# Optimization experiments

Hardware: AMD Instinct MI355X
Metric: run time of the kernel (lower is better)

## Reference

```python
import jax, jax.numpy as jnp
import numpy as np

N_NODES = 20000
N_EDGES = 320000
N_GRAPHS = 128


def gat_conv(x, W, attn_l, attn_r, bias, src, dst, num_nodes):
    """DGL-style GATConv: per-edge attention, edge softmax over incoming
    edges of each destination node, scatter-sum aggregation."""
    H, D = attn_l.shape
    feat = (x @ W).reshape(-1, H, D)                      # [N,H,D]
    el = jnp.sum(feat * attn_l, axis=-1)                  # [N,H]
    er = jnp.sum(feat * attn_r, axis=-1)                  # [N,H]
    e = jax.nn.leaky_relu(el[src] + er[dst], 0.2)         # [E,H]
    # numerically stable segment softmax over dst
    m = jax.ops.segment_max(e, dst, num_segments=num_nodes)   # [N,H]
    e_exp = jnp.exp(e - m[dst])                               # [E,H]
    denom = jax.ops.segment_sum(e_exp, dst, num_segments=num_nodes)
    alpha = e_exp / denom[dst]                                 # [E,H]
    msg = alpha[:, :, None] * feat[src]                        # [E,H,D]
    rst = jax.ops.segment_sum(msg, dst, num_segments=num_nodes)  # [N,H,D]
    return rst + bias.reshape(1, H, D)


def setup_inputs() -> dict:
    key = jax.random.key(0)
    ks = jax.random.split(key, 12)
    s1 = 1.0 / np.sqrt(256.0)
    s2 = 1.0 / np.sqrt(512.0)
    return {
        "x": jax.random.normal(ks[0], (N_NODES, 256), dtype=jnp.float32),
        "W1": jax.random.normal(ks[1], (256, 512), dtype=jnp.float32) * s1,
        "a_l1": jax.random.normal(ks[2], (8, 64), dtype=jnp.float32) * 0.1,
        "a_r1": jax.random.normal(ks[3], (8, 64), dtype=jnp.float32) * 0.1,
        "b1": jnp.zeros((512,), dtype=jnp.float32),
        "W2": jax.random.normal(ks[4], (512, 128), dtype=jnp.float32) * s2,
        "a_l2": jax.random.normal(ks[5], (1, 128), dtype=jnp.float32) * 0.1,
        "a_r2": jax.random.normal(ks[6], (1, 128), dtype=jnp.float32) * 0.1,
        "b2": jnp.zeros((128,), dtype=jnp.float32),
        "edge_src": jax.random.randint(ks[7], (N_EDGES,), 0, N_NODES, dtype=jnp.int32),
        "edge_dst": jax.random.randint(ks[8], (N_EDGES,), 0, N_NODES, dtype=jnp.int32),
        "graph_ids": jnp.sort(jax.random.randint(ks[9], (N_NODES,), 0, N_GRAPHS, dtype=jnp.int32)),
    }


def reference(x, W1, a_l1, a_r1, b1, W2, a_l2, a_r2, b2, edge_src, edge_dst, graph_ids):
    h = gat_conv(x, W1, a_l1, a_r1, b1, edge_src, edge_dst, N_NODES)  # [N,8,64]
    h = h.reshape(N_NODES, -1)                                        # flatten(1)
    h = gat_conv(h, W2, a_l2, a_r2, b2, edge_src, edge_dst, N_NODES)  # [N,1,128]
    # dgl.mean_nodes: per-graph mean pooling
    ones = jnp.ones((N_NODES,), dtype=h.dtype)
    counts = jax.ops.segment_sum(ones, graph_ids, num_segments=N_GRAPHS)
    sums = jax.ops.segment_sum(h, graph_ids, num_segments=N_GRAPHS)   # [G,1,128]
    hg = sums / jnp.maximum(counts, 1.0)[:, None, None]
    return hg
```

## Files before the change

kernel.cpp:

```cpp
#include <hip/hip_runtime.h>
#include <hip/hip_fp16.h>

#define N_NODES  20000
#define N_EDGES  320000
#define N_GRAPHS 128

typedef _Float16 half8 __attribute__((ext_vector_type(8)));
typedef float    f32x4 __attribute__((ext_vector_type(4)));

__global__ void setup_hist(const float* __restrict__ W1, const float* __restrict__ W2,
                           __half* __restrict__ w1t, __half* __restrict__ w2t,
                           const int* __restrict__ gid, int* __restrict__ gstart,
                           const int* __restrict__ dst, int* __restrict__ deg) {
    const int tid  = blockIdx.x * blockDim.x + threadIdx.x;
    const int nthr = gridDim.x * blockDim.x;
    for (int i = tid; i < 256 * 512; i += nthr) {
        int r = i >> 9, c = i & 511;
        w1t[c * 256 + r] = __float2half(W1[i]);
    }
    for (int i = tid; i < 512 * 128; i += nthr) {
        int r = i >> 7, c = i & 127;
        w2t[c * 512 + r] = __float2half(W2[i]);
    }
    if (tid <= N_GRAPHS) {
        if (tid == N_GRAPHS) gstart[N_GRAPHS] = N_NODES;
        else {
            int lo = 0, hi = N_NODES;
            while (lo < hi) {
                int mid = (lo + hi) >> 1;
                if (gid[mid] < tid) lo = mid + 1; else hi = mid;
            }
            gstart[tid] = lo;
        }
    }
    for (int e = tid; e < N_EDGES; e += nthr) atomicAdd(&deg[dst[e]], 1);
}

__global__ void scan_kernel(const int* __restrict__ deg, int* __restrict__ rowptr, int n) {
    __shared__ int partial[1024];
    const int t = threadIdx.x;
    const int CH = (n + 1023) / 1024;
    const int base = t * CH;
    int local = 0;
    for (int i = 0; i < CH; ++i)
        if (base + i < n) local += deg[base + i];
    partial[t] = local;
    __syncthreads();
    for (int o = 1; o < 1024; o <<= 1) {
        int v = (t >= o) ? partial[t - o] : 0;
        __syncthreads();
        partial[t] += v;
        __syncthreads();
    }
    int run = (t == 0) ? 0 : partial[t - 1];
    for (int i = 0; i < CH; ++i) {
        if (base + i <= n) rowptr[base + i] = run;
        if (base + i < n) run += deg[base + i];
    }
}

template <int BM, int BN, int WM, int WN, int H, int D, bool AF32>
__device__ __forceinline__ void gemm_body(
        int bx, int by,
        const void* __restrict__ A_, const __half* __restrict__ BT,
        __half* __restrict__ C, const float* __restrict__ al,
        const float* __restrict__ ar, float* __restrict__ el,
        float* __restrict__ er, int Mm, int Nn, int Kk) {
    constexpr int BK  = 32;
    constexpr int MFR = WM / 16, NFR = WN / 16;
    constexpr int WCOLS = BN / WN;
    __shared__ __align__(16) __half As[BM * BK];
    __shared__ __align__(16) __half Bs[BN * BK];
    const int tid  = threadIdx.x;
    const int w    = tid >> 6, lane = tid & 63;
    const int wr   = w / WCOLS, wc = w % WCOLS;
    const int brow = bx * BM;
    const int bcol = by * BN;
    const int lr   = lane & 15;
    const int lk   = (lane >> 4) * 8;

    f32x4 acc[MFR][NFR] = {};

    for (int k0 = 0; k0 < Kk; k0 += BK) {
        for (int c = tid; c < BM * 4; c += 256) {
            int r = c >> 2, ko = (c & 3) * 8;
            int gr = brow + r; if (gr >= Mm) gr = Mm - 1;
            int off = (r * BK + ko) ^ ((r & 7) << 3);
            if constexpr (AF32) {
                const float* ap = (const float*)A_ + (size_t)gr * Kk + k0 + ko;
                float4 v0 = *reinterpret_cast<const float4*>(ap);
                float4 v1 = *reinterpret_cast<const float4*>(ap + 4);
                union { __half2 h2[4]; uint4 u; } pk;
                pk.h2[0] = __floats2half2_rn(v0.x, v0.y);
                pk.h2[1] = __floats2half2_rn(v0.z, v0.w);
                pk.h2[2] = __floats2half2_rn(v1.x, v1.y);
                pk.h2[3] = __floats2half2_rn(v1.z, v1.w);
                *reinterpret_cast<uint4*>(&As[off]) = pk.u;
            } else {
                *reinterpret_cast<uint4*>(&As[off]) =
                    *reinterpret_cast<const uint4*>((const __half*)A_ + (size_t)gr * Kk + k0 + ko);
            }
        }
        for (int c = tid; c < BN * 4; c += 256) {
            int r = c >> 2, ko = (c & 3) * 8;
            int off = (r * BK + ko) ^ ((r & 7) << 3);
            *reinterpret_cast<uint4*>(&Bs[off]) =
                *reinterpret_cast<const uint4*>(&BT[(size_t)(bcol + r) * Kk + k0 + ko]);
        }
        __syncthreads();
        half8 af[MFR], bf[NFR];
#pragma unroll
        for (int m = 0; m < MFR; ++m) {
            int r = wr * WM + m * 16 + lr;
            af[m] = *reinterpret_cast<const half8*>(&As[(r * BK + lk) ^ ((r & 7) << 3)]);
        }
#pragma unroll
        for (int n = 0; n < NFR; ++n) {
            int r = wc * WN + n * 16 + lr;
            bf[n] = *reinterpret_cast<const half8*>(&Bs[(r * BK + lk) ^ ((r & 7) << 3)]);
        }
#pragma unroll
        for (int m = 0; m < MFR; ++m)
#pragma unroll
            for (int n = 0; n < NFR; ++n)
                acc[m][n] = __builtin_amdgcn_mfma_f32_16x16x32_f16(af[m], bf[n], acc[m][n], 0, 0, 0);
        __syncthreads();
    }

#pragma unroll
    for (int m = 0; m < MFR; ++m) {
        int r0 = brow + wr * WM + m * 16 + ((lane >> 4) << 2);
#pragma unroll
        for (int n = 0; n < NFR; ++n) {
            int cc = bcol + wc * WN + n * 16 + lr;
#pragma unroll
            for (int g = 0; g < 4; ++g)
                if (r0 + g < Mm) C[(size_t)(r0 + g) * Nn + cc] = __float2half(acc[m][n][g]);
        }
    }
    const int h = (bcol + wc * WN) / D;
    float alv[NFR], arv[NFR];
#pragma unroll
    for (int n = 0; n < NFR; ++n) {
        alv[n] = al[bcol + wc * WN + n * 16 + lr];
        arv[n] = ar[bcol + wc * WN + n * 16 + lr];
    }
#pragma unroll
    for (int m = 0; m < MFR; ++m) {
#pragma unroll
        for (int g = 0; g < 4; ++g) {
            float pl = 0.f, pr = 0.f;
#pragma unroll
            for (int n = 0; n < NFR; ++n) {
                pl += acc[m][n][g] * alv[n];
                pr += acc[m][n][g] * arv[n];
            }
            pl += __shfl_xor(pl, 1); pl += __shfl_xor(pl, 2);
            pl += __shfl_xor(pl, 4); pl += __shfl_xor(pl, 8);
            pr += __shfl_xor(pr, 1); pr += __shfl_xor(pr, 2);
            pr += __shfl_xor(pr, 4); pr += __shfl_xor(pr, 8);
            int gr = brow + wr * WM + m * 16 + ((lane >> 4) << 2) + g;
            if (lr == 0 && gr < Mm) {
                if constexpr (WN == D) {
                    el[(size_t)gr * H + h] = pl;
                    er[(size_t)gr * H + h] = pr;
                } else {
                    atomicAdd(&el[(size_t)gr * H + h], pl);
                    atomicAdd(&er[(size_t)gr * H + h], pr);
                }
            }
        }
    }
}

template <int BM, int BN, int WM, int WN, int H, int D, bool AF32>
__global__ __launch_bounds__(256) void gemm_kernel(
        const void* __restrict__ A_, const __half* __restrict__ BT,
        __half* __restrict__ C, const float* __restrict__ al,
        const float* __restrict__ ar, float* __restrict__ el,
        float* __restrict__ er, int Mm, int Nn, int Kk) {
    gemm_body<BM, BN, WM, WN, H, D, AF32>(blockIdx.x, blockIdx.y, A_, BT, C,
                                          al, ar, el, er, Mm, Nn, Kk);
}

template <int BM, int BN, int WM, int WN, int H, int D, bool AF32>
__global__ __launch_bounds__(256) void gemm_scatter_kernel(
        const void* __restrict__ A_, const __half* __restrict__ BT,
        __half* __restrict__ C, const float* __restrict__ al,
        const float* __restrict__ ar, float* __restrict__ el,
        float* __restrict__ er, int Mm, int Nn, int Kk, int gemmRows,
        const int* __restrict__ src, const int* __restrict__ dst,
        const int* __restrict__ rowptr, int* __restrict__ cursor,
        int* __restrict__ esrc) {
    const int nbGemm = gemmRows * (Nn / BN);
    if ((int)blockIdx.x < nbGemm) {
        gemm_body<BM, BN, WM, WN, H, D, AF32>(blockIdx.x % gemmRows, blockIdx.x / gemmRows,
                                              A_, BT, C, al, ar, el, er, Mm, Nn, Kk);
    } else {
        int e = (blockIdx.x - nbGemm) * blockDim.x + threadIdx.x;
        if (e < N_EDGES) {
            int d = dst[e];
            int pos = rowptr[d] + atomicAdd(&cursor[d], 1);
            esrc[pos] = src[e];
        }
    }
}

template <int F, int H, bool HOUT>
__global__ __launch_bounds__(256) void node_aggr_wave(
        const __half* __restrict__ feat, const float* __restrict__ el,
        const float* __restrict__ er, const int* __restrict__ rowptr,
        const int* __restrict__ esrc, const float* __restrict__ bias,
        void* __restrict__ rst_, int N) {
    constexpr int LPN = F / 8;
    constexpr int NPW = 64 / LPN;
    constexpr int D   = F / H;
    const int wid  = (blockIdx.x * blockDim.x + threadIdx.x) >> 6;
    const int lane = threadIdx.x & 63;
    const int n    = wid * NPW + lane / LPN;
    if (n >= N) return;
    const int col = (lane % LPN) * 8;
    const int h   = col / D;
    const float ern = er[(size_t)n * H + h];
    const int rs = rowptr[n], re = rowptr[n + 1];
    const __half* fq = feat + col;

    float acc[8] = {};
    float dsum = 0.f;
    int i = rs;
    for (; i + 4 <= re; i += 4) {
        int s0 = esrc[i], s1 = esrc[i + 1], s2 = esrc[i + 2], s3 = esrc[i + 3];
        float x0 = el[(size_t)s0 * H + h] + ern;
        float x1 = el[(size_t)s1 * H + h] + ern;
        float x2 = el[(size_t)s2 * H + h] + ern;
        float x3 = el[(size_t)s3 * H + h] + ern;
        x0 = (x0 > 0.f) ? x0 : 0.2f * x0;
        x1 = (x1 > 0.f) ? x1 : 0.2f * x1;
        x2 = (x2 > 0.f) ? x2 : 0.2f * x2;
        x3 = (x3 > 0.f) ? x3 : 0.2f * x3;
        float w0 = __expf(x0), w1 = __expf(x1), w2 = __expf(x2), w3 = __expf(x3);
        union { uint4 u; __half2 h2[4]; } r0, r1, r2, r3;
        r0.u = *reinterpret_cast<const uint4*>(fq + (size_t)s0 * F);
        r1.u = *reinterpret_cast<const uint4*>(fq + (size_t)s1 * F);
        r2.u = *reinterpret_cast<const uint4*>(fq + (size_t)s2 * F);
        r3.u = *reinterpret_cast<const uint4*>(fq + (size_t)s3 * F);
        dsum += (w0 + w1) + (w2 + w3);
#pragma unroll
        for (int k = 0; k < 4; ++k) {
            float2 f0 = __half22float2(r0.h2[k]);
            float2 f1 = __half22float2(r1.h2[k]);
            float2 f2 = __half22float2(r2.h2[k]);
            float2 f3 = __half22float2(r3.h2[k]);
            acc[2 * k]     += w0 * f0.x + w1 * f1.x + w2 * f2.x + w3 * f3.x;
            acc[2 * k + 1] += w0 * f0.y + w1 * f1.y + w2 * f2.y + w3 * f3.y;
        }
    }
    for (; i < re; ++i) {
        int s = esrc[i];
        float x = el[(size_t)s * H + h] + ern;
        x = (x > 0.f) ? x : 0.2f * x;
        float w = __expf(x);
        union { uint4 u; __half2 h2[4]; } r;
        r.u = *reinterpret_cast<const uint4*>(fq + (size_t)s * F);
        dsum += w;
#pragma unroll
        for (int k = 0; k < 4; ++k) {
            float2 f = __half22float2(r.h2[k]);
            acc[2 * k]     += w * f.x;
            acc[2 * k + 1] += w * f.y;
        }
    }
    float inv = (re > rs) ? 1.f / dsum : 0.f;
    float4 b0 = *reinterpret_cast<const float4*>(bias + col);
    float4 b1 = *reinterpret_cast<const float4*>(bias + col + 4);
    float o[8] = {acc[0] * inv + b0.x, acc[1] * inv + b0.y,
                  acc[2] * inv + b0.z, acc[3] * inv + b0.w,
                  acc[4] * inv + b1.x, acc[5] * inv + b1.y,
                  acc[6] * inv + b1.z, acc[7] * inv + b1.w};
    if constexpr (HOUT) {
        union { __half2 h2[4]; uint4 u; } pk;
        pk.h2[0] = __floats2half2_rn(o[0], o[1]);
        pk.h2[1] = __floats2half2_rn(o[2], o[3]);
        pk.h2[2] = __floats2half2_rn(o[4], o[5]);
        pk.h2[3] = __floats2half2_rn(o[6], o[7]);
        *reinterpret_cast<uint4*>((__half*)rst_ + (size_t)n * F + col) = pk.u;
    } else {
        float* op = (float*)rst_ + (size_t)n * F + col;
        *reinterpret_cast<float4*>(op)     = make_float4(o[0], o[1], o[2], o[3]);
        *reinterpret_cast<float4*>(op + 4) = make_float4(o[4], o[5], o[6], o[7]);
    }
}

__global__ __launch_bounds__(1024) void seg_pool_kernel(
        const float* __restrict__ h, const int* __restrict__ start,
        float* __restrict__ out, int D) {
    __shared__ float part[7][128];
    int g = blockIdx.x;
    int d = threadIdx.x & 127;
    int j = threadIdx.x >> 7;
    int s = start[g], e = start[g + 1];
    float acc = 0.f;
    for (int n = s + j; n < e; n += 8) acc += h[(size_t)n * D + d];
    if (j > 0) part[j - 1][d] = acc;
    __syncthreads();
    if (j == 0) {
#pragma unroll
        for (int k = 0; k < 7; ++k) acc += part[k][d];
        out[(size_t)g * D + d] = acc / fmaxf((float)(e - s), 1.f);
    }
}

extern "C" void kernel_launch(void* const* d_in, const int* in_sizes, int n_in,
                              void* d_out, int out_size, void* d_ws, size_t ws_size,
                              hipStream_t stream) {
    const float* x   = (const float*)d_in[0];
    const float* W1  = (const float*)d_in[1];
    const float* al1 = (const float*)d_in[2];
    const float* ar1 = (const float*)d_in[3];
    const float* b1  = (const float*)d_in[4];
    const float* W2  = (const float*)d_in[5];
    const float* al2 = (const float*)d_in[6];
    const float* ar2 = (const float*)d_in[7];
    const float* b2  = (const float*)d_in[8];
    const int* src   = (const int*)d_in[9];
    const int* dst   = (const int*)d_in[10];
    const int* gid   = (const int*)d_in[11];
    float* out = (float*)d_out;

    float* ws = (float*)d_ws;
    size_t off = 0;
    int* deg    = (int*)(ws + off); off += N_NODES;
    int* cursor = (int*)(ws + off); off += N_NODES;
    int* rowptr = (int*)(ws + off); off += N_NODES + 4;
    int* gstart = (int*)(ws + off); off += N_GRAPHS + 4;
    int* esrc   = (int*)(ws + off); off += N_EDGES;
    __half* w1t    = (__half*)(ws + off); off += 512 * 256 / 2;
    __half* w2t    = (__half*)(ws + off); off += 128 * 512 / 2;
    __half* feat1h = (__half*)(ws + off); off += (size_t)N_NODES * 256;
    float*  el1    = ws + off; off += (size_t)N_NODES * 8;
    float*  er1    = ws + off; off += (size_t)N_NODES * 8;
    __half* rst1h  = (__half*)(ws + off); off += (size_t)N_NODES * 256;
    __half* feat2h = (__half*)(ws + off); off += (size_t)N_NODES * 64;
    float*  el2    = ws + off; off += N_NODES;
    float*  er2    = ws + off; off += N_NODES;
    float*  rst2   = ws + off; off += (size_t)N_NODES * 128;

    hipMemsetAsync(deg, 0, sizeof(int) * 2 * N_NODES, stream);

    setup_hist<<<(N_EDGES + 255) / 256, 256, 0, stream>>>(
        W1, W2, w1t, w2t, gid, gstart, dst, deg);
    scan_kernel<<<1, 1024, 0, stream>>>(deg, rowptr, N_NODES);

    const int g1rows = (N_NODES + 127) / 128;
    const int g1nb   = g1rows * (512 / 128);
    const int scb    = (N_EDGES + 255) / 256;
    gemm_scatter_kernel<128, 128, 64, 64, 8, 64, true><<<g1nb + scb, 256, 0, stream>>>(
        x, w1t, feat1h, al1, ar1, el1, er1, N_NODES, 512, 256, g1rows,
        src, dst, rowptr, cursor, esrc);
    node_aggr_wave<512, 8, true><<<(N_NODES * 64 + 255) / 256, 256, 0, stream>>>(
        feat1h, el1, er1, rowptr, esrc, b1, rst1h, N_NODES);

    dim3 g2((N_NODES + 63) / 64, 1);
    gemm_kernel<64, 128, 16, 128, 1, 128, false><<<g2, 256, 0, stream>>>(
        rst1h, w2t, feat2h, al2, ar2, el2, er2, N_NODES, 128, 512);
    node_aggr_wave<128, 1, false><<<(N_NODES * 16 + 255) / 256, 256, 0, stream>>>(
        feat2h, el2, er2, rowptr, esrc, b2, rst2, N_NODES);

    seg_pool_kernel<<<N_GRAPHS, 1024, 0, stream>>>(rst2, gstart, out, 128);
}
```

Baseline: 181.8 us.

## Remap GEMM block order for XCD locality and store layer-2 output in half

The fused GEMM-plus-scatter kernel now assigns consecutive block IDs (mod 8) to different row tiles, grouping row tiles per column so each XCD works on neighbouring rows and can reuse A-tiles in its L2. The row count is padded to a multiple of 8, which adds idle blocks. Separately, the layer-2 aggregation now writes fp16 instead of fp32, and the pooling kernel reads half values. This halves that intermediate's memory traffic but adds rounding before the mean.

```diff
diff --git a/kernel.cpp b/kernel.cpp
--- a/kernel.cpp
+++ b/kernel.cpp
@@ -183,7 +183,7 @@
                                           al, ar, el, er, Mm, Nn, Kk);
 }
 
-template <int BM, int BN, int WM, int WN, int H, int D, bool AF32>
+template <int BM, int BN, int WM, int WN, int H, int D, bool AF32, int NCOL>
 __global__ __launch_bounds__(256) void gemm_scatter_kernel(
         const void* __restrict__ A_, const __half* __restrict__ BT,
         __half* __restrict__ C, const float* __restrict__ al,
@@ -192,12 +192,19 @@
         const int* __restrict__ src, const int* __restrict__ dst,
         const int* __restrict__ rowptr, int* __restrict__ cursor,
         int* __restrict__ esrc) {
-    const int nbGemm = gemmRows * (Nn / BN);
-    if ((int)blockIdx.x < nbGemm) {
-        gemm_body<BM, BN, WM, WN, H, D, AF32>(blockIdx.x % gemmRows, blockIdx.x / gemmRows,
-                                              A_, BT, C, al, ar, el, er, Mm, Nn, Kk);
+    const int rowsPad = ((gemmRows + 7) >> 3) << 3;
+    const int nbGemm  = rowsPad * NCOL;
+    const int bid = blockIdx.x;
+    if (bid < nbGemm) {
+        int slot = bid & 7;
+        int c    = (bid >> 3) % NCOL;
+        int grp  = bid / (8 * NCOL);
+        int r    = grp * 8 + slot;
+        if (r < gemmRows)
+            gemm_body<BM, BN, WM, WN, H, D, AF32>(r, c, A_, BT, C,
+                                                  al, ar, el, er, Mm, Nn, Kk);
     } else {
-        int e = (blockIdx.x - nbGemm) * blockDim.x + threadIdx.x;
+        int e = (bid - nbGemm) * blockDim.x + threadIdx.x;
         if (e < N_EDGES) {
             int d = dst[e];
             int pos = rowptr[d] + atomicAdd(&cursor[d], 1);
@@ -292,7 +299,7 @@
 }
 
 __global__ __launch_bounds__(1024) void seg_pool_kernel(
-        const float* __restrict__ h, const int* __restrict__ start,
+        const __half* __restrict__ h, const int* __restrict__ start,
         float* __restrict__ out, int D) {
     __shared__ float part[7][128];
     int g = blockIdx.x;
@@ -300,7 +307,7 @@
     int j = threadIdx.x >> 7;
     int s = start[g], e = start[g + 1];
     float acc = 0.f;
-    for (int n = s + j; n < e; n += 8) acc += h[(size_t)n * D + d];
+    for (int n = s + j; n < e; n += 8) acc += __half2float(h[(size_t)n * D + d]);
     if (j > 0) part[j - 1][d] = acc;
     __syncthreads();
     if (j == 0) {
@@ -343,7 +350,7 @@
     __half* feat2h = (__half*)(ws + off); off += (size_t)N_NODES * 64;
     float*  el2    = ws + off; off += N_NODES;
     float*  er2    = ws + off; off += N_NODES;
-    float*  rst2   = ws + off; off += (size_t)N_NODES * 128;
+    __half* rst2h  = (__half*)(ws + off); off += (size_t)N_NODES * 64;
 
     hipMemsetAsync(deg, 0, sizeof(int) * 2 * N_NODES, stream);
 
@@ -351,10 +358,11 @@
         W1, W2, w1t, w2t, gid, gstart, dst, deg);
     scan_kernel<<<1, 1024, 0, stream>>>(deg, rowptr, N_NODES);
 
-    const int g1rows = (N_NODES + 127) / 128;
-    const int g1nb   = g1rows * (512 / 128);
-    const int scb    = (N_EDGES + 255) / 256;
-    gemm_scatter_kernel<128, 128, 64, 64, 8, 64, true><<<g1nb + scb, 256, 0, stream>>>(
+    const int g1rows   = (N_NODES + 127) / 128;
+    const int rowsPad  = ((g1rows + 7) / 8) * 8;
+    const int g1nb     = rowsPad * 4;
+    const int scb      = (N_EDGES + 255) / 256;
+    gemm_scatter_kernel<128, 128, 64, 64, 8, 64, true, 4><<<g1nb + scb, 256, 0, stream>>>(
         x, w1t, feat1h, al1, ar1, el1, er1, N_NODES, 512, 256, g1rows,
         src, dst, rowptr, cursor, esrc);
     node_aggr_wave<512, 8, true><<<(N_NODES * 64 + 255) / 256, 256, 0, stream>>>(
@@ -363,8 +371,8 @@
     dim3 g2((N_NODES + 63) / 64, 1);
     gemm_kernel<64, 128, 16, 128, 1, 128, false><<<g2, 256, 0, stream>>>(
         rst1h, w2t, feat2h, al2, ar2, el2, er2, N_NODES, 128, 512);
-    node_aggr_wave<128, 1, false><<<(N_NODES * 16 + 255) / 256, 256, 0, stream>>>(
-        feat2h, el2, er2, rowptr, esrc, b2, rst2, N_NODES);
-
-    seg_pool_kernel<<<N_GRAPHS, 1024, 0, stream>>>(rst2, gstart, out, 128);
-}
+    node_aggr_wave<128, 1, true><<<(N_NODES * 16 + 255) / 256, 256, 0, stream>>>(
+        feat2h, el2, er2, rowptr, esrc, b2, rst2h, N_NODES);
+
+    seg_pool_kernel<<<N_GRAPHS, 1024, 0, stream>>>(rst2h, gstart, out, 128);
+}
```

After: 176.4 us. 1.03x faster.
